# Kernel optimization log

Measured on AMD Instinct MI355X. Metric: run time of the kernel, lower is better.

The kernel has to match this reference:

```python
import jax, jax.numpy as jnp
import numpy as np

B, S, L, D = 128, 256, 200, 768
POS_VOCAB, POS_DIM = 60, 50
REDUC, HID, TAGS, POL = 400, 150, 5, 4


def setup_inputs() -> dict:
    key = jax.random.key(0)
    ks = jax.random.split(key, 12)
    bert_vectors = jax.random.normal(ks[0], (B, S, D), dtype=jnp.float32)
    # ragged subword spans: word j covers subwords [start_j, end_j] (inclusive), length 1..3,
    # skipping the [CLS] token at index 0. Clipped to S-1 (long sentences just truncate).
    rng = np.random.default_rng(0)
    lens = rng.integers(1, 4, size=(B, L))
    cum = np.cumsum(lens, axis=1)
    starts = 1 + cum - lens
    ends = cum
    starts = np.minimum(starts, S - 1)
    ends = np.minimum(ends, S - 1)
    ends = np.maximum(ends, starts)
    positions = jnp.asarray(np.stack([starts, ends], axis=-1), dtype=jnp.int32)
    postag = jax.random.randint(ks[1], (B, L), 1, POS_VOCAB).astype(jnp.int32)

    def lin(k, o, i):
        return jax.random.normal(k, (o, i), jnp.float32) / np.float32(np.sqrt(i))

    return dict(
        bert_vectors=bert_vectors,
        positions=positions,
        postag=postag,
        embed_table=jax.random.normal(ks[2], (POS_VOCAB, POS_DIM), jnp.float32) * 0.02,
        W_reduc=lin(ks[3], REDUC, D + POS_DIM), b_reduc=jnp.zeros((REDUC,), jnp.float32),
        W_ap=lin(ks[4], HID, REDUC), b_ap=jnp.zeros((HID,), jnp.float32),
        W_op=lin(ks[5], HID, REDUC), b_op=jnp.zeros((HID,), jnp.float32),
        W_ap2=lin(ks[6], HID, REDUC), b_ap2=jnp.zeros((HID,), jnp.float32),
        W_op2=lin(ks[7], HID, REDUC), b_op2=jnp.zeros((HID,), jnp.float32),
        W_aptag=lin(ks[8], TAGS, HID), b_aptag=jnp.zeros((TAGS,), jnp.float32),
        W_optag=lin(ks[9], TAGS, HID), b_optag=jnp.zeros((TAGS,), jnp.float32),
        W_bi=lin(ks[10], POL * HID, HID + 1),
    )


def _pool_subwords(vectors, positions):
    # variable-length mean pooling of subword vectors into word vectors
    # vectors: [B,S,D], positions: [B,L,2] -> [B,L,D]
    idx = jnp.arange(S)[None, None, :]                      # [1,1,S]
    p0 = positions[..., 0][..., None]                       # [B,L,1]
    p1 = positions[..., 1][..., None]
    m = ((idx >= p0) & (idx <= p1)).astype(vectors.dtype)   # [B,L,S]
    cnt = jnp.maximum(m.sum(-1, keepdims=True), 1.0)
    return jnp.einsum('bls,bsd->bld', m, vectors) / cnt


def reference(bert_vectors, positions, postag, embed_table,
              W_reduc, b_reduc, W_ap, b_ap, W_op, b_op,
              W_ap2, b_ap2, W_op2, b_op2,
              W_aptag, b_aptag, W_optag, b_optag, W_bi):
    word_vecs = _pool_subwords(bert_vectors, positions)                 # [B,L,D]
    pos_emb = embed_table[postag]                                       # [B,L,50]
    h = jnp.concatenate([pos_emb, word_vecs], axis=-1)                  # [B,L,D+50]
    reduc = jnp.einsum('blf,of->blo', h, W_reduc) + b_reduc             # [B,L,400]
    ap_rep = jax.nn.relu(jnp.einsum('blf,of->blo', reduc, W_ap) + b_ap)
    op_rep = jax.nn.relu(jnp.einsum('blf,of->blo', reduc, W_op) + b_op)
    ap_node = jax.nn.relu(jnp.einsum('blf,of->blo', reduc, W_ap2) + b_ap2)
    op_node = jax.nn.relu(jnp.einsum('blf,of->blo', reduc, W_op2) + b_op2)
    ap_out = jnp.einsum('blf,of->blo', ap_rep, W_aptag) + b_aptag       # [B,L,5]
    op_out = jnp.einsum('blf,of->blo', op_rep, W_optag) + b_optag       # [B,L,5]
    # Biaffine(150,150,POL,bias=(True,False))
    ones = jnp.ones((B, L, 1), ap_node.dtype)
    in1 = jnp.concatenate([ap_node, ones], axis=-1)                     # [B,L,151]
    affine = jnp.einsum('bli,oi->blo', in1, W_bi).reshape(B, L * POL, HID)
    tri = jnp.einsum('bkh,bmh->bkm', affine, op_node)                   # [B,L*POL,L]
    triplet_out = tri.transpose(0, 2, 1).reshape(B, L, L, POL)          # [B,L2,L1,POL]
    return (ap_out, op_out, triplet_out)
```

## Files before the change

kernel.cpp:

```cpp
#include <hip/hip_runtime.h>
#include <hip/hip_bf16.h>

#define Bsz 128
#define Ssz 256
#define Lsz 200
#define Dsz 768
#define POS_DIM 50
#define TAGS 5
#define NROW 25600
#define FIN 818
#define KH 832
#define KR 416
#define KD 160

typedef __attribute__((ext_vector_type(8))) short short8;
typedef __attribute__((ext_vector_type(4))) short short4v;
typedef __attribute__((ext_vector_type(4))) float floatx4;

__device__ __forceinline__ short f2bf(float v) {
    __hip_bfloat16 h = __float2bfloat16(v);
    short s; __builtin_memcpy(&s, &h, 2); return s;
}
__device__ __forceinline__ float bf2f(short s) {
    __hip_bfloat16 h; __builtin_memcpy(&h, &s, 2);
    return __bfloat162float(h);
}

__device__ __forceinline__ void gload16(const short* g, short* l) {
    __builtin_amdgcn_global_load_lds(
        (const __attribute__((address_space(1))) void*)g,
        (__attribute__((address_space(3))) void*)l, 16, 0, 0);
}

__global__ void prep_kernel(const float* __restrict__ W_reduc,
                            const float* __restrict__ W_ap, const float* __restrict__ W_op,
                            const float* __restrict__ W_ap2, const float* __restrict__ W_op2,
                            const float* __restrict__ W_bi,
                            const float* __restrict__ b_reduc,
                            const float* __restrict__ b_ap, const float* __restrict__ b_op,
                            const float* __restrict__ b_ap2, const float* __restrict__ b_op2,
                            short* __restrict__ Wr_bf, short* __restrict__ Wh_bf,
                            short* __restrict__ Wbi_bf,
                            float* __restrict__ br_pad, float* __restrict__ bh_pad,
                            float* __restrict__ bbi_pad)
{
    int i = blockIdx.x * blockDim.x + threadIdx.x;
    if (i < 512 * KH) {
        int r = i / KH, k = i % KH;
        float v = 0.0f;
        if (r < 400) {
            if (k < 768)       v = W_reduc[r * FIN + POS_DIM + k];
            else if (k < 818)  v = W_reduc[r * FIN + (k - 768)];
        }
        Wr_bf[i] = f2bf(v);
    }
    if (i < 640 * KR) {
        int r = i / KR, c = i % KR;
        float v = 0.0f;
        if (r < 600 && c < 400) {
            const float* src = (r < 150) ? W_ap : (r < 300) ? W_op : (r < 450) ? W_ap2 : W_op2;
            v = src[(r % 150) * 400 + c];
        }
        Wh_bf[i] = f2bf(v);
    }
    if (i < 640 * KD) {
        int r = i / KD, c = i % KD;
        Wbi_bf[i] = (r < 600 && c < 150) ? f2bf(W_bi[r * 151 + c]) : (short)0;
    }
    if (i < KR) br_pad[i] = (i < 400) ? b_reduc[i] : 0.0f;
    if (i < 640) {
        float v = 0.0f;
        if (i < 600) {
            const float* bs = (i < 150) ? b_ap : (i < 300) ? b_op : (i < 450) ? b_ap2 : b_op2;
            v = bs[i % 150];
        }
        bh_pad[i] = v;
        bbi_pad[i] = (i < 600) ? W_bi[i * 151 + 150] : 0.0f;
    }
}

__global__ __launch_bounds__(256) void pool_kernel(
    const float* __restrict__ bert,
    const int* __restrict__ positions,
    const int* __restrict__ postag,
    const float* __restrict__ embed,
    short* __restrict__ h_bf)
{
    int row = blockIdx.x;
    int b = row / Lsz;
    int st = positions[row * 2 + 0];
    int en = positions[row * 2 + 1];
    int tag = postag[row];
    int span = en - st + 1;
    float inv = 1.0f / (float)span;
    const float* base = bert + ((long)b * Ssz + st) * Dsz;
    short* hr = h_bf + (long)row * KH;

    int t = threadIdx.x;
    int c0 = t * 4;
    if (c0 >= KH) return;
    short4v o;
    if (c0 < 768) {
        float4 s = {0.f, 0.f, 0.f, 0.f};
        for (int i = 0; i < span; ++i) {
            float4 v = *(const float4*)(base + i * Dsz + c0);
            s.x += v.x; s.y += v.y; s.z += v.z; s.w += v.w;
        }
        o.x = f2bf(s.x * inv); o.y = f2bf(s.y * inv);
        o.z = f2bf(s.z * inv); o.w = f2bf(s.w * inv);
    } else {
        const float* e = embed + tag * POS_DIM;
#pragma unroll
        for (int j = 0; j < 4; ++j) {
            int c = c0 + j - 768;
            float v = (c < POS_DIM) ? e[c] : 0.0f;
            ((short*)&o)[j] = f2bf(v);
        }
    }
    *(short4v*)(hr + c0) = o;
}

__global__ __launch_bounds__(256) void gemm_mfma(
    const short* __restrict__ A, long long sAb, int lda,
    const short* __restrict__ Bt, long long sBb, int ldb,
    const float* __restrict__ bias,
    short* __restrict__ outB, float* __restrict__ outF, long long sCb, int ldc,
    int M, int Nv, int K, int mode)
{
    __shared__ __align__(16) short AB[8192];

    int bz = blockIdx.z;
    A += (long long)bz * sAb;
    Bt += (long long)bz * sBb;

    int row0 = blockIdx.y * 128;
    int col0 = blockIdx.x * 128;
    int tid = threadIdx.x;
    int lane = tid & 63;
    int wv = tid >> 6;
    int lm = lane & 15, lk = lane >> 4;
    int wr = (wv >> 1) * 64;
    int wc = (wv & 1) * 64;

    int c0 = tid, c1 = tid + 256;
    const short* gA0 = A + (long)(row0 + (c0 & 127)) * lda + (c0 >> 7) * 8;
    const short* gA1 = A + (long)(row0 + (c1 & 127)) * lda + (c1 >> 7) * 8;
    const short* gB0 = Bt + (long)(col0 + (c0 & 127)) * ldb + (c0 >> 7) * 8;
    const short* gB1 = Bt + (long)(col0 + (c1 & 127)) * ldb + (c1 >> 7) * 8;
    short* lA0 = &AB[c0 * 8];
    short* lA1 = &AB[c1 * 8];
    short* lB0 = &AB[4096 + c0 * 8];
    short* lB1 = &AB[4096 + c1 * 8];

    const short* fA = &AB[(lk * 128 + wr + lm) * 8];
    const short* fB = &AB[4096 + (lk * 128 + wc + lm) * 8];

    floatx4 acc[4][4];
#pragma unroll
    for (int i = 0; i < 4; ++i)
#pragma unroll
        for (int j = 0; j < 4; ++j)
            acc[i][j] = (floatx4){0.f, 0.f, 0.f, 0.f};

    for (int k0 = 0; k0 < K; k0 += 32) {
        gload16(gA0 + k0, lA0);
        gload16(gA1 + k0, lA1);
        gload16(gB0 + k0, lB0);
        gload16(gB1 + k0, lB1);
        __syncthreads();
        short8 a[4], b[4];
#pragma unroll
        for (int mt = 0; mt < 4; ++mt) a[mt] = *(const short8*)(fA + mt * 128);
#pragma unroll
        for (int nt = 0; nt < 4; ++nt) b[nt] = *(const short8*)(fB + nt * 128);
#pragma unroll
        for (int mt = 0; mt < 4; ++mt)
#pragma unroll
            for (int nt = 0; nt < 4; ++nt)
                acc[mt][nt] = __builtin_amdgcn_mfma_f32_16x16x32_bf16(
                    a[mt], b[nt], acc[mt][nt], 0, 0, 0);
        __syncthreads();
    }

#pragma unroll
    for (int mt = 0; mt < 4; ++mt) {
#pragma unroll
        for (int nt = 0; nt < 4; ++nt) {
#pragma unroll
            for (int r = 0; r < 4; ++r) {
                int gm = row0 + wr + mt * 16 + lk * 4 + r;
                int gn = col0 + wc + nt * 16 + lm;
                float v = acc[mt][nt][r];
                if (mode == 0) {
                    if (gn < Nv)
                        outB[(long)gm * ldc + gn] = f2bf(v + bias[gn]);
                } else if (mode == 1) {
                    if (gn < 600) {
                        v = fmaxf(v + bias[gn], 0.0f);
                        outB[((long)(gn / 150) * NROW + gm) * KD + gn % 150] = f2bf(v);
                    } else if (gn < 640) {
                        int q = gn - 600;
                        outB[((long)(q / 10) * NROW + gm) * KD + 150 + q % 10] = 0;
                    }
                } else if (mode == 2) {
                    int bb = gm / 200, l = gm % 200;
                    if (gn < 600) {
                        v += bias[gn];
                        outB[((long)bb * 800 + l * 4 + gn / 150) * KD + gn % 150] = f2bf(v);
                    } else if (gn < 640) {
                        int q = gn - 600;
                        outB[((long)bb * 800 + l * 4 + q / 10) * KD + 150 + q % 10] = 0;
                    }
                } else {
                    if (gm < M && gn < Nv)
                        outF[(long long)bz * sCb + (long)gm * ldc + gn] = v;
                }
            }
        }
    }
}

__global__ __launch_bounds__(256) void tags_kernel(
    const short* __restrict__ hid4,
    const float* __restrict__ W_aptag, const float* __restrict__ b_aptag,
    const float* __restrict__ W_optag, const float* __restrict__ b_optag,
    float* __restrict__ out_ap, float* __restrict__ out_op)
{
    int wave = threadIdx.x / 64;
    int lane = threadIdx.x % 64;
    int row = blockIdx.x * 4 + wave;
    if (row >= NROW) return;

#pragma unroll
    for (int which = 0; which < 2; ++which) {
        const short* rep = hid4 + ((long)which * NROW + row) * KD;
        const float* W = which ? W_optag : W_aptag;
        const float* bb = which ? b_optag : b_aptag;
        float* out = which ? out_op : out_ap;
        float v0 = bf2f(rep[lane]);
        float v1 = bf2f(rep[64 + lane]);
        float v2 = (lane < 22) ? bf2f(rep[128 + lane]) : 0.0f;
#pragma unroll
        for (int t = 0; t < TAGS; ++t) {
            const float* w = W + t * 150;
            float p = v0 * w[lane] + v1 * w[64 + lane] +
                      ((lane < 22) ? v2 * w[128 + lane] : 0.0f);
#pragma unroll
            for (int off = 32; off > 0; off >>= 1) p += __shfl_down(p, off);
            if (lane == 0) out[row * TAGS + t] = p + bb[t];
        }
    }
}

extern "C" void kernel_launch(void* const* d_in, const int* in_sizes, int n_in,
                              void* d_out, int out_size, void* d_ws, size_t ws_size,
                              hipStream_t stream)
{
    const float* bert      = (const float*)d_in[0];
    const int*   positions = (const int*)d_in[1];
    const int*   postag    = (const int*)d_in[2];
    const float* embed     = (const float*)d_in[3];
    const float* W_reduc   = (const float*)d_in[4];
    const float* b_reduc   = (const float*)d_in[5];
    const float* W_ap      = (const float*)d_in[6];
    const float* b_ap      = (const float*)d_in[7];
    const float* W_op      = (const float*)d_in[8];
    const float* b_op      = (const float*)d_in[9];
    const float* W_ap2     = (const float*)d_in[10];
    const float* b_ap2     = (const float*)d_in[11];
    const float* W_op2     = (const float*)d_in[12];
    const float* b_op2     = (const float*)d_in[13];
    const float* W_aptag   = (const float*)d_in[14];
    const float* b_aptag   = (const float*)d_in[15];
    const float* W_optag   = (const float*)d_in[16];
    const float* b_optag   = (const float*)d_in[17];
    const float* W_bi      = (const float*)d_in[18];

    float* out = (float*)d_out;
    float* out_ap  = out;
    float* out_op  = out + NROW * TAGS;
    float* out_tri = out + 2 * NROW * TAGS;

    short* ws = (short*)d_ws;
    short* h_bf     = ws;
    short* affine   = h_bf;
    short* reduc_bf = h_bf + (long)NROW * KH;
    short* hid4     = reduc_bf + (long)NROW * KR;
    short* Wr_bf    = hid4 + (long)4 * NROW * KD;
    short* Wh_bf    = Wr_bf + 512 * KH;
    short* Wbi_bf   = Wh_bf + 640 * KR;
    float* br_pad   = (float*)(Wbi_bf + 640 * KD);
    float* bh_pad   = br_pad + KR;
    float* bbi_pad  = bh_pad + 640;

    prep_kernel<<<(512 * KH + 255) / 256, 256, 0, stream>>>(
        W_reduc, W_ap, W_op, W_ap2, W_op2, W_bi,
        b_reduc, b_ap, b_op, b_ap2, b_op2,
        Wr_bf, Wh_bf, Wbi_bf, br_pad, bh_pad, bbi_pad);

    pool_kernel<<<NROW, 256, 0, stream>>>(bert, positions, postag, embed, h_bf);

    {
        dim3 g(4, NROW / 128, 1);
        gemm_mfma<<<g, 256, 0, stream>>>(h_bf, 0, KH, Wr_bf, 0, KH, br_pad,
                                         reduc_bf, nullptr, 0, KR,
                                         NROW, KR, KH, 0);
    }
    {
        dim3 g(5, NROW / 128, 1);
        gemm_mfma<<<g, 256, 0, stream>>>(reduc_bf, 0, KR, Wh_bf, 0, KR, bh_pad,
                                         hid4, nullptr, 0, 0,
                                         NROW, 600, KR, 1);
    }
    tags_kernel<<<NROW / 4, 256, 0, stream>>>(hid4, W_aptag, b_aptag,
                                              W_optag, b_optag, out_ap, out_op);
    {
        dim3 g(5, NROW / 128, 1);
        gemm_mfma<<<g, 256, 0, stream>>>(hid4 + (long)2 * NROW * KD, 0, KD,
                                         Wbi_bf, 0, KD, bbi_pad,
                                         affine, nullptr, 0, 0,
                                         NROW, 600, KD, 2);
    }
    {
        dim3 g(7, 2, Bsz);
        gemm_mfma<<<g, 256, 0, stream>>>(hid4 + (long)3 * NROW * KD, (long long)200 * KD, KD,
                                         affine, (long long)800 * KD, KD, nullptr,
                                         nullptr, out_tri, (long long)200 * 800, 800,
                                         200, 800, KD, 3);
    }
}
```

Measured before the change: 477.5 us.

## Double-buffer LDS tiles in MFMA GEMM to overlap loads with compute

The single LDS buffer in the GEMM k-loop becomes two buffers. The next k-tile's global-to-LDS load is issued before computing on the current tile, and one of the two barriers per iteration is removed. The aim is to hide global load latency behind the MFMA work. In exchange, LDS use per block doubles to 32KB, which may reduce occupancy, and correctness depends on gload16's completion semantics before the barrier.

```diff
diff --git a/kernel.cpp b/kernel.cpp
--- a/kernel.cpp
+++ b/kernel.cpp
@@ -127,7 +127,7 @@
     short* __restrict__ outB, float* __restrict__ outF, long long sCb, int ldc,
     int M, int Nv, int K, int mode)
 {
-    __shared__ __align__(16) short AB[8192];
+    __shared__ __align__(16) short AB[16384];
 
     int bz = blockIdx.z;
     A += (long long)bz * sAb;
@@ -147,13 +147,6 @@
     const short* gA1 = A + (long)(row0 + (c1 & 127)) * lda + (c1 >> 7) * 8;
     const short* gB0 = Bt + (long)(col0 + (c0 & 127)) * ldb + (c0 >> 7) * 8;
     const short* gB1 = Bt + (long)(col0 + (c1 & 127)) * ldb + (c1 >> 7) * 8;
-    short* lA0 = &AB[c0 * 8];
-    short* lA1 = &AB[c1 * 8];
-    short* lB0 = &AB[4096 + c0 * 8];
-    short* lB1 = &AB[4096 + c1 * 8];
-
-    const short* fA = &AB[(lk * 128 + wr + lm) * 8];
-    const short* fB = &AB[4096 + (lk * 128 + wc + lm) * 8];
 
     floatx4 acc[4][4];
 #pragma unroll
@@ -162,25 +155,40 @@
         for (int j = 0; j < 4; ++j)
             acc[i][j] = (floatx4){0.f, 0.f, 0.f, 0.f};
 
-    for (int k0 = 0; k0 < K; k0 += 32) {
-        gload16(gA0 + k0, lA0);
-        gload16(gA1 + k0, lA1);
-        gload16(gB0 + k0, lB0);
-        gload16(gB1 + k0, lB1);
-        __syncthreads();
+    auto stage = [&](int buf, int koff) {
+        short* base = &AB[buf * 8192];
+        gload16(gA0 + koff, base + c0 * 8);
+        gload16(gA1 + koff, base + c1 * 8);
+        gload16(gB0 + koff, base + 4096 + c0 * 8);
+        gload16(gB1 + koff, base + 4096 + c1 * 8);
+    };
+    auto compute = [&](int buf) {
+        const short* fa = &AB[buf * 8192 + (lk * 128 + wr + lm) * 8];
+        const short* fb = &AB[buf * 8192 + 4096 + (lk * 128 + wc + lm) * 8];
         short8 a[4], b[4];
 #pragma unroll
-        for (int mt = 0; mt < 4; ++mt) a[mt] = *(const short8*)(fA + mt * 128);
-#pragma unroll
-        for (int nt = 0; nt < 4; ++nt) b[nt] = *(const short8*)(fB + nt * 128);
+        for (int mt = 0; mt < 4; ++mt) a[mt] = *(const short8*)(fa + mt * 128);
+#pragma unroll
+        for (int nt = 0; nt < 4; ++nt) b[nt] = *(const short8*)(fb + nt * 128);
 #pragma unroll
         for (int mt = 0; mt < 4; ++mt)
 #pragma unroll
             for (int nt = 0; nt < 4; ++nt)
                 acc[mt][nt] = __builtin_amdgcn_mfma_f32_16x16x32_bf16(
                     a[mt], b[nt], acc[mt][nt], 0, 0, 0);
+    };
+
+    int nt = K >> 5;
+    stage(0, 0);
+    __syncthreads();
+    int cur = 0;
+    for (int t = 0; t + 1 < nt; ++t) {
+        stage(cur ^ 1, (t + 1) << 5);
+        compute(cur);
         __syncthreads();
-    }
+        cur ^= 1;
+    }
+    compute(cur);
 
 #pragma unroll
     for (int mt = 0; mt < 4; ++mt) {
```

New measurement: 478.8 us. Within noise of the previous version (+0.3%).
